# Optimization experiments

Measured on AMD Instinct MI355X. Metric: run time of the kernel, lower is better.

Reference implementation:

```python
import jax, jax.numpy as jnp
import numpy as np

B, C, IMG, P = 64, 3, 224, 16
GRID = IMG // P          # 14
N = GRID * GRID          # 196 patch tokens
D = 768
L, H = 12, 12
HD = D // H              # 64
FF = 4 * D               # 3072
NC = 1000
PRUNE_LAYER = 6
KEEP = max(1, int(N * 0.5))  # 98 tokens kept after pruning
LN_EPS = 1e-6


def _ln(x, g, b):
    m = jnp.mean(x, axis=-1, keepdims=True)
    v = jnp.var(x, axis=-1, keepdims=True)
    return (x - m) * jax.lax.rsqrt(v + LN_EPS) * g + b


def _block(x, g1, b1, qw, qb, pw, pb, g2, b2, w1, c1, w2, c2):
    # standard timm ViT block: x + Attn(LN(x)); x + MLP(LN(x))
    Bq, S, _ = x.shape
    h = _ln(x, g1, b1)
    qkv = (h @ qw + qb).reshape(Bq, S, 3, H, HD)
    q, k, v = qkv[:, :, 0], qkv[:, :, 1], qkv[:, :, 2]  # [B,S,H,HD]
    attn = jax.nn.softmax(jnp.einsum('bqhd,bkhd->bhqk', q, k) * (HD ** -0.5), axis=-1)
    o = jnp.einsum('bhqk,bkhd->bqhd', attn, v).reshape(Bq, S, D)
    x = x + o @ pw + pb
    h = _ln(x, g2, b2)
    return x + jax.nn.gelu(h @ w1 + c1, approximate=False) @ w2 + c2


def _forward(x, patch_w, patch_b, cls_token, pos_embed, ln1_g, ln1_b, qkv_w, qkv_b,
             proj_w, proj_b, ln2_g, ln2_b, fc1_w, fc1_b, fc2_w, fc2_b,
             norm_g, norm_b, head_w, head_b):
    Bq = x.shape[0]
    # patch embed: conv(k=16, s=16) == patchify + linear; flatten order (C, ph, pw) matches torch conv weight layout
    patches = x.reshape(Bq, C, GRID, P, GRID, P).transpose(0, 2, 4, 1, 3, 5).reshape(Bq, N, C * P * P)
    t = patches @ patch_w + patch_b                                     # [B,N,D]
    t = jnp.concatenate([jnp.broadcast_to(cls_token, (Bq, 1, D)), t], axis=1) + pos_embed  # [B,197,D]

    blk = lambda t, i: _block(t, ln1_g[i], ln1_b[i], qkv_w[i], qkv_b[i], proj_w[i], proj_b[i],
                              ln2_g[i], ln2_b[i], fc1_w[i], fc1_b[i], fc2_w[i], fc2_b[i])
    for i in range(PRUNE_LAYER):
        t = blk(t, i)

    cls_tok, patch_tok = t[:, :1], t[:, 1:]
    # per-token L2 scores + topk selection + gather (the irregular-access stage)
    scores = jnp.sqrt(jnp.sum(patch_tok * patch_tok, axis=-1))          # [B,N]
    _, idx = jax.lax.top_k(scores, KEEP)                                # sorted descending, matches torch.topk
    sel = jnp.take_along_axis(patch_tok, idx[:, :, None], axis=1)       # [B,K,D]
    t = jnp.concatenate([cls_tok, sel], axis=1)                         # [B,K+1,D]

    for i in range(PRUNE_LAYER, L):
        t = blk(t, i)
    t = _ln(t, norm_g, norm_b)
    return t[:, 0] @ head_w + head_b                                    # [B,NC]


def setup_inputs() -> dict:
    key = jax.random.key(0)
    ks = jax.random.split(key, 12)
    s = 0.02
    f32 = jnp.float32
    return {
        'x': jax.random.normal(ks[0], (B, C, IMG, IMG), f32),
        'patch_w': jax.random.normal(ks[1], (C * P * P, D), f32) * s,
        'patch_b': jnp.zeros((D,), f32),
        'cls_token': jax.random.normal(ks[2], (1, 1, D), f32) * s,
        'pos_embed': jax.random.normal(ks[3], (1, N + 1, D), f32) * s,
        'ln1_g': jnp.ones((L, D), f32), 'ln1_b': jnp.zeros((L, D), f32),
        'qkv_w': jax.random.normal(ks[4], (L, D, 3 * D), f32) * s,
        'qkv_b': jnp.zeros((L, 3 * D), f32),
        'proj_w': jax.random.normal(ks[5], (L, D, D), f32) * s,
        'proj_b': jnp.zeros((L, D), f32),
        'ln2_g': jnp.ones((L, D), f32), 'ln2_b': jnp.zeros((L, D), f32),
        'fc1_w': jax.random.normal(ks[6], (L, D, FF), f32) * s,
        'fc1_b': jnp.zeros((L, FF), f32),
        'fc2_w': jax.random.normal(ks[7], (L, FF, D), f32) * s,
        'fc2_b': jnp.zeros((L, D), f32),
        'norm_g': jnp.ones((D,), f32), 'norm_b': jnp.zeros((D,), f32),
        'head_w': jax.random.normal(ks[8], (D, NC), f32) * s,
        'head_b': jnp.zeros((NC,), f32),
    }


def reference(x, patch_w, patch_b, cls_token, pos_embed, ln1_g, ln1_b, qkv_w, qkv_b,
              proj_w, proj_b, ln2_g, ln2_b, fc1_w, fc1_b, fc2_w, fc2_b,
              norm_g, norm_b, head_w, head_b):
    return _forward(x, patch_w, patch_b, cls_token, pos_embed, ln1_g, ln1_b, qkv_w, qkv_b,
                    proj_w, proj_b, ln2_g, ln2_b, fc1_w, fc1_b, fc2_w, fc2_b,
                    norm_g, norm_b, head_w, head_b)
```

## Files before the change

kernel.cpp:

```cpp
#include <hip/hip_runtime.h>
#include <hip/hip_bf16.h>
#include <cstddef>
#include <cstdint>

namespace {

constexpr int B = 64, CIN = 3, IMG = 224, PS = 16, GRID_ = 14, NPATCH = 196;
constexpr int D = 768, H = 12, HD = 64, FFD = 3072, NC = 1000;
constexpr int S1 = 197, S2 = 99, KEEP = 98, PRUNE = 6, LAYERS = 12;
constexpr float LN_EPS = 1e-6f;

typedef __attribute__((ext_vector_type(8))) short bf16x8;
typedef __attribute__((ext_vector_type(4))) float f32x4;

__device__ inline float wave_red_sum(float v) {
  #pragma unroll
  for (int off = 32; off > 0; off >>= 1) v += __shfl_xor(v, off, 64);
  return v;
}

__device__ inline void gl16(const __hip_bfloat16* g, __hip_bfloat16* l) {
  __builtin_amdgcn_global_load_lds(
      (const __attribute__((address_space(1))) void*)g,
      (__attribute__((address_space(3))) void*)l,
      16, 0, 0);
}

__global__ __launch_bounds__(256) void tcvt_k(const float* __restrict__ src,
                                              __hip_bfloat16* __restrict__ dst,
                                              int R, int C, size_t lstride) {
  src += (size_t)blockIdx.z * lstride;
  dst += (size_t)blockIdx.z * lstride;
  __shared__ float tile[32][33];
  int c0 = blockIdx.x * 32, r0 = blockIdx.y * 32;
  int tx = threadIdx.x & 31, ty = threadIdx.x >> 5;
  #pragma unroll
  for (int i = 0; i < 32; i += 8) {
    int r = r0 + ty + i, c = c0 + tx;
    tile[ty + i][tx] = (r < R && c < C) ? src[(size_t)r * C + c] : 0.f;
  }
  __syncthreads();
  #pragma unroll
  for (int i = 0; i < 32; i += 8) {
    int c = c0 + ty + i, r = r0 + tx;
    if (c < C && r < R) dst[(size_t)c * R + r] = __float2bfloat16(tile[tx][ty + i]);
  }
}

__global__ void patchify_k(const float* __restrict__ x, __hip_bfloat16* __restrict__ out) {
  size_t idx = (size_t)blockIdx.x * blockDim.x + threadIdx.x;
  size_t total = (size_t)B * NPATCH * D;
  if (idx >= total) return;
  int row = (int)(idx / D), k = (int)(idx % D);
  int b = row / NPATCH, n = row % NPATCH;
  int gr = n / GRID_, gc = n % GRID_;
  int c = k / (PS * PS), rr = (k % (PS * PS)) / PS, cc = k % PS;
  out[idx] = __float2bfloat16(x[((size_t)(b * CIN + c) * IMG + (gr * PS + rr)) * IMG + gc * PS + cc]);
}

template <int MODE>
__global__ __launch_bounds__(256) void bgemm_k(
    const __hip_bfloat16* __restrict__ A, const __hip_bfloat16* __restrict__ BT,
    const float* __restrict__ bias, void* __restrict__ Cc,
    int M, int N, int K, const float* __restrict__ extra) {
  __shared__ __hip_bfloat16 As[128 * 32];
  __shared__ __hip_bfloat16 Bs[128 * 32];
  int tid = threadIdx.x, lane = tid & 63, wv = tid >> 6;
  int wr = wv >> 1, wc = wv & 1;
  int m0 = blockIdx.y * 128, n0 = blockIdx.x * 128;
  int fr = lane & 15, fq = lane >> 4;
  int srow0 = wv * 32 + (lane >> 2);
  int skk = (lane & 3) * 8;
  f32x4 acc[4][4] = {};
  for (int k0 = 0; k0 < K; k0 += 32) {
    #pragma unroll
    for (int i = 0; i < 2; ++i) {
      int r = srow0 + i * 16;
      int gra = m0 + r; gra = (gra < M) ? gra : (M - 1);
      gl16(A + (size_t)gra * K + k0 + skk, &As[r * 32 + skk]);
      int grb = n0 + r; grb = (grb < N) ? grb : (N - 1);
      gl16(BT + (size_t)grb * K + k0 + skk, &Bs[r * 32 + skk]);
    }
    __syncthreads();
    bf16x8 af[4], bg[4];
    #pragma unroll
    for (int m = 0; m < 4; ++m) af[m] = *(const bf16x8*)&As[(wr * 64 + m * 16 + fr) * 32 + fq * 8];
    #pragma unroll
    for (int n = 0; n < 4; ++n) bg[n] = *(const bf16x8*)&Bs[(wc * 64 + n * 16 + fr) * 32 + fq * 8];
    #pragma unroll
    for (int m = 0; m < 4; ++m)
      #pragma unroll
      for (int n = 0; n < 4; ++n)
        acc[m][n] = __builtin_amdgcn_mfma_f32_16x16x32_bf16(af[m], bg[n], acc[m][n], 0, 0, 0);
    __syncthreads();
  }
  #pragma unroll
  for (int m = 0; m < 4; ++m) {
    #pragma unroll
    for (int n = 0; n < 4; ++n) {
      #pragma unroll
      for (int j = 0; j < 4; ++j) {
        int row = m0 + wr * 64 + m * 16 + fq * 4 + j;
        int col = n0 + wc * 64 + n * 16 + fr;
        if (row >= M || col >= N) continue;
        float v = acc[m][n][j] + bias[col];
        if (MODE == 0) {
          ((__hip_bfloat16*)Cc)[(size_t)row * N + col] = __float2bfloat16(v);
        } else if (MODE == 1) {
          int b = row / NPATCH, nn = row % NPATCH;
          ((float*)Cc)[((size_t)(b * S1 + 1 + nn)) * D + col] = v + extra[(size_t)(1 + nn) * D + col];
        } else if (MODE == 2) {
          ((float*)Cc)[(size_t)row * N + col] += v;
        } else {
          float g = 0.5f * v * (1.0f + erff(v * 0.7071067811865476f));
          ((__hip_bfloat16*)Cc)[(size_t)row * N + col] = __float2bfloat16(g);
        }
      }
    }
  }
}

__global__ __launch_bounds__(256) void gemm_k(
    const float* __restrict__ A, const float* __restrict__ Bw,
    const float* __restrict__ bias, float* __restrict__ Cc,
    int M, int N, int K) {
  __shared__ float As[64][17];
  __shared__ float Bs[16][64];
  int tid = threadIdx.x;
  int tx = tid & 15, ty = tid >> 4;
  int m0 = blockIdx.y * 64, n0 = blockIdx.x * 64;
  float acc[4][4] = {};
  for (int k0 = 0; k0 < K; k0 += 16) {
    #pragma unroll
    for (int j = 0; j < 4; ++j) {
      int i = tid + 256 * j;
      int r = i >> 4, c = i & 15;
      int gr = m0 + r;
      As[r][c] = (gr < M) ? A[(size_t)gr * K + (k0 + c)] : 0.f;
    }
    #pragma unroll
    for (int j = 0; j < 4; ++j) {
      int i = tid + 256 * j;
      int r = i >> 6, c = i & 63;
      int gc = n0 + c;
      Bs[r][c] = (gc < N) ? Bw[(size_t)(k0 + r) * N + gc] : 0.f;
    }
    __syncthreads();
    #pragma unroll
    for (int kk = 0; kk < 16; ++kk) {
      float a[4], bb[4];
      #pragma unroll
      for (int ii = 0; ii < 4; ++ii) a[ii] = As[ty * 4 + ii][kk];
      #pragma unroll
      for (int jj = 0; jj < 4; ++jj) bb[jj] = Bs[kk][tx * 4 + jj];
      #pragma unroll
      for (int ii = 0; ii < 4; ++ii)
        #pragma unroll
        for (int jj = 0; jj < 4; ++jj) acc[ii][jj] = fmaf(a[ii], bb[jj], acc[ii][jj]);
    }
    __syncthreads();
  }
  #pragma unroll
  for (int ii = 0; ii < 4; ++ii) {
    int row = m0 + ty * 4 + ii;
    if (row >= M) continue;
    #pragma unroll
    for (int jj = 0; jj < 4; ++jj) {
      int col = n0 + tx * 4 + jj;
      if (col >= N) continue;
      Cc[(size_t)row * N + col] = acc[ii][jj] + bias[col];
    }
  }
}

__global__ void cls_init_k(float* __restrict__ t, const float* __restrict__ cls,
                           const float* __restrict__ pos) {
  int idx = blockIdx.x * blockDim.x + threadIdx.x;
  if (idx >= B * D) return;
  int b = idx / D, d = idx % D;
  t[(size_t)b * S1 * D + d] = cls[d] + pos[d];
}

template <typename OutT>
__global__ __launch_bounds__(256) void ln_k(const float* __restrict__ in, OutT* __restrict__ out,
                                            const float* __restrict__ g, const float* __restrict__ bta,
                                            size_t istride, size_t ostride) {
  int row = blockIdx.x;
  const float* p = in + (size_t)row * istride;
  int tid = threadIdx.x;
  float v0 = p[tid], v1 = p[tid + 256], v2 = p[tid + 512];
  float s = v0 + v1 + v2;
  float s2 = v0 * v0 + v1 * v1 + v2 * v2;
  s = wave_red_sum(s);
  s2 = wave_red_sum(s2);
  __shared__ float r1[4], r2[4];
  int lane = tid & 63, w = tid >> 6;
  if (lane == 0) { r1[w] = s; r2[w] = s2; }
  __syncthreads();
  s = r1[0] + r1[1] + r1[2] + r1[3];
  s2 = r2[0] + r2[1] + r2[2] + r2[3];
  float mean = s * (1.0f / 768.0f);
  float var = s2 * (1.0f / 768.0f) - mean * mean;
  float rs = rsqrtf(var + LN_EPS);
  OutT* q = out + (size_t)row * ostride;
  #pragma unroll
  for (int c = 0; c < 3; ++c) {
    int i = tid + 256 * c;
    float vv = (c == 0 ? v0 : (c == 1 ? v1 : v2));
    float r = (vv - mean) * rs * g[i] + bta[i];
    if constexpr (sizeof(OutT) == 2) q[i] = __float2bfloat16(r);
    else q[i] = r;
  }
}

template <int NT16>
__global__ __launch_bounds__(256) void attn3_k(const __hip_bfloat16* __restrict__ qkv,
                                               __hip_bfloat16* __restrict__ o, int S) {
  constexpr int NT32 = (NT16 + 1) / 2;
  constexpr int COLS = NT32 * 32;
  constexpr int STR = COLS + 8;
  __shared__ __hip_bfloat16 VT[64 * STR];
  __shared__ __hip_bfloat16 P[4][16 * STR];
  int bh = blockIdx.x;
  int b = bh / H, hh = bh % H;
  int tid = threadIdx.x, lane = tid & 63, wv = tid >> 6;
  int fr = lane & 15, fq = lane >> 4;
  const size_t rs = 3 * D;
  const __hip_bfloat16* qb = qkv + ((size_t)b * S) * rs + hh * HD;
  const __hip_bfloat16* kb = qb + D;
  const __hip_bfloat16* vb = qb + 2 * D;
  const __hip_bfloat16 z = __float2bfloat16(0.f);
  for (int idx = tid; idx < COLS * 64; idx += 256) {
    int key = idx >> 6, d = idx & 63;
    VT[d * STR + key] = (key < S) ? vb[(size_t)key * rs + d] : z;
  }
  if (NT16 & 1) {
    for (int idx = lane; idx < 16 * 16; idx += 64)
      P[wv][(idx >> 4) * STR + NT16 * 16 + (idx & 15)] = z;
  }
  __syncthreads();

  for (int qt = wv; qt * 16 < S; qt += 4) {
    int q0 = qt * 16;
    int qrow = q0 + fr;
    const __hip_bfloat16* qp = qb + (size_t)(qrow < S ? qrow : 0) * rs + fq * 8;
    bf16x8 aq0 = *(const bf16x8*)(qp);
    bf16x8 aq1 = *(const bf16x8*)(qp + 32);
    f32x4 sc[NT16];
    #pragma unroll
    for (int kt = 0; kt < NT16; ++kt) {
      int krow = kt * 16 + fr;
      const __hip_bfloat16* kp = kb + (size_t)(krow < S ? krow : 0) * rs + fq * 8;
      bf16x8 bk0 = *(const bf16x8*)(kp);
      bf16x8 bk1 = *(const bf16x8*)(kp + 32);
      f32x4 a = {};
      a = __builtin_amdgcn_mfma_f32_16x16x32_bf16(aq0, bk0, a, 0, 0, 0);
      a = __builtin_amdgcn_mfma_f32_16x16x32_bf16(aq1, bk1, a, 0, 0, 0);
      sc[kt] = a;
    }
    float lj[4];
    #pragma unroll
    for (int jj = 0; jj < 4; ++jj) {
      float mx = -1e30f;
      #pragma unroll
      for (int kt = 0; kt < NT16; ++kt) {
        float v = sc[kt][jj] * 0.125f;
        if (kt * 16 + fr >= S) v = -1e30f;
        sc[kt][jj] = v;
        mx = fmaxf(mx, v);
      }
      mx = fmaxf(mx, __shfl_xor(mx, 1, 64));
      mx = fmaxf(mx, __shfl_xor(mx, 2, 64));
      mx = fmaxf(mx, __shfl_xor(mx, 4, 64));
      mx = fmaxf(mx, __shfl_xor(mx, 8, 64));
      float sum = 0.f;
      #pragma unroll
      for (int kt = 0; kt < NT16; ++kt) {
        float p = __expf(sc[kt][jj] - mx);
        sc[kt][jj] = p;
        sum += p;
      }
      sum += __shfl_xor(sum, 1, 64);
      sum += __shfl_xor(sum, 2, 64);
      sum += __shfl_xor(sum, 4, 64);
      sum += __shfl_xor(sum, 8, 64);
      lj[jj] = 1.0f / sum;
    }
    __hip_bfloat16* pw = &P[wv][0];
    #pragma unroll
    for (int kt = 0; kt < NT16; ++kt)
      #pragma unroll
      for (int jj = 0; jj < 4; ++jj)
        pw[(fq * 4 + jj) * STR + kt * 16 + fr] = __float2bfloat16(sc[kt][jj]);
    #pragma unroll
    for (int dt = 0; dt < 4; ++dt) {
      f32x4 oa = {};
      #pragma unroll
      for (int kc = 0; kc < NT32; ++kc) {
        bf16x8 ap = *(const bf16x8*)&pw[fr * STR + kc * 32 + fq * 8];
        bf16x8 bv = *(const bf16x8*)&VT[(dt * 16 + fr) * STR + kc * 32 + fq * 8];
        oa = __builtin_amdgcn_mfma_f32_16x16x32_bf16(ap, bv, oa, 0, 0, 0);
      }
      #pragma unroll
      for (int jj = 0; jj < 4; ++jj) {
        int orow = q0 + fq * 4 + jj;
        if (orow < S)
          o[((size_t)(b * S + orow)) * D + hh * HD + dt * 16 + fr] =
              __float2bfloat16(oa[jj] * lj[jj]);
      }
    }
  }
}

__global__ void score_k(const float* __restrict__ t, float* __restrict__ scores) {
  int gw = (blockIdx.x * blockDim.x + threadIdx.x) >> 6;
  int lane = threadIdx.x & 63;
  if (gw >= B * NPATCH) return;
  int b = gw / NPATCH, n = gw % NPATCH;
  const float* p = t + ((size_t)(b * S1) + 1 + n) * D;
  float a = 0.f;
  #pragma unroll
  for (int j = lane; j < D; j += 64) { float v = p[j]; a += v * v; }
  a = wave_red_sum(a);
  if (lane == 0) scores[gw] = sqrtf(a);
}

__global__ __launch_bounds__(256) void select_k(const float* __restrict__ scores, int* __restrict__ map) {
  int b = blockIdx.x;
  __shared__ float s[NPATCH];
  __shared__ int flag[NPATCH];
  int i = threadIdx.x;
  if (i < NPATCH) s[i] = scores[b * NPATCH + i];
  __syncthreads();
  if (i < NPATCH) {
    float si = s[i];
    int r = 0;
    for (int j = 0; j < NPATCH; ++j) {
      float sj = s[j];
      r += (sj > si) || (sj == si && j < i);
    }
    flag[i] = (r < KEEP) ? 1 : 0;
  }
  __syncthreads();
  if (i < NPATCH && flag[i]) {
    int p = 0;
    for (int j = 0; j < i; ++j) p += flag[j];
    map[b * (KEEP + 1) + 1 + p] = 1 + i;
  }
  if (i == 0) map[b * (KEEP + 1)] = 0;
}

__global__ void gather_k(const float* __restrict__ t, const int* __restrict__ map,
                         float* __restrict__ t2) {
  int br = blockIdx.x;
  int b = br / S2;
  int src = map[br];
  const float* p = t + ((size_t)b * S1 + src) * D;
  float* q = t2 + (size_t)br * D;
  for (int j = threadIdx.x; j < D; j += blockDim.x) q[j] = p[j];
}

}

extern "C" void kernel_launch(void* const* d_in, const int* in_sizes, int n_in,
                              void* d_out, int out_size, void* d_ws, size_t ws_size,
                              hipStream_t stream) {
  const float* x       = (const float*)d_in[0];
  const float* patch_w = (const float*)d_in[1];
  const float* patch_b = (const float*)d_in[2];
  const float* cls_tok = (const float*)d_in[3];
  const float* pos_emb = (const float*)d_in[4];
  const float* ln1_g   = (const float*)d_in[5];
  const float* ln1_b   = (const float*)d_in[6];
  const float* qkv_w   = (const float*)d_in[7];
  const float* qkv_b   = (const float*)d_in[8];
  const float* proj_w  = (const float*)d_in[9];
  const float* proj_b  = (const float*)d_in[10];
  const float* ln2_g   = (const float*)d_in[11];
  const float* ln2_b   = (const float*)d_in[12];
  const float* fc1_w   = (const float*)d_in[13];
  const float* fc1_b   = (const float*)d_in[14];
  const float* fc2_w   = (const float*)d_in[15];
  const float* fc2_b   = (const float*)d_in[16];
  const float* norm_g  = (const float*)d_in[17];
  const float* norm_b  = (const float*)d_in[18];
  const float* head_w  = (const float*)d_in[19];
  const float* head_b  = (const float*)d_in[20];
  float* out = (float*)d_out;

  char* wp = (char*)d_ws;
  auto alloc = [&](size_t bytes) { char* r = wp; wp += (bytes + 255) & ~(size_t)255; return r; };
  float* t   = (float*)alloc((size_t)B * S1 * D * 4);
  float* t2  = (float*)alloc((size_t)B * S2 * D * 4);
  float* hf  = (float*)alloc((size_t)B * D * 4);
  float* scores = (float*)alloc((size_t)B * NPATCH * 4);
  int*   map    = (int*)alloc((size_t)B * S2 * 4);
  __hip_bfloat16* h   = (__hip_bfloat16*)alloc((size_t)B * S1 * D * 2);
  __hip_bfloat16* qkv = (__hip_bfloat16*)alloc((size_t)B * S1 * 3 * D * 2);
  __hip_bfloat16* ff  = (__hip_bfloat16*)alloc((size_t)B * S1 * FFD * 2);
  __hip_bfloat16* qkvT  = (__hip_bfloat16*)alloc((size_t)LAYERS * 3 * D * D * 2);
  __hip_bfloat16* projT = (__hip_bfloat16*)alloc((size_t)LAYERS * D * D * 2);
  __hip_bfloat16* fc1T  = (__hip_bfloat16*)alloc((size_t)LAYERS * FFD * D * 2);
  __hip_bfloat16* fc2T  = (__hip_bfloat16*)alloc((size_t)LAYERS * D * FFD * 2);
  __hip_bfloat16* patchT = (__hip_bfloat16*)alloc((size_t)D * D * 2);
  __hip_bfloat16* patches = ff;

  { dim3 g(3 * D / 32, D / 32, LAYERS);
    tcvt_k<<<g, 256, 0, stream>>>(qkv_w, qkvT, D, 3 * D, (size_t)D * 3 * D); }
  { dim3 g(D / 32, D / 32, LAYERS);
    tcvt_k<<<g, 256, 0, stream>>>(proj_w, projT, D, D, (size_t)D * D); }
  { dim3 g(FFD / 32, D / 32, LAYERS);
    tcvt_k<<<g, 256, 0, stream>>>(fc1_w, fc1T, D, FFD, (size_t)D * FFD); }
  { dim3 g(D / 32, FFD / 32, LAYERS);
    tcvt_k<<<g, 256, 0, stream>>>(fc2_w, fc2T, FFD, D, (size_t)FFD * D); }
  { dim3 g(D / 32, D / 32, 1);
    tcvt_k<<<g, 256, 0, stream>>>(patch_w, patchT, D, D, 0); }

  {
    size_t total = (size_t)B * NPATCH * D;
    patchify_k<<<(unsigned)((total + 255) / 256), 256, 0, stream>>>(x, patches);
    dim3 g(D / 128, (B * NPATCH) / 128);
    bgemm_k<1><<<g, 256, 0, stream>>>(patches, patchT, patch_b, t, B * NPATCH, D, D, pos_emb);
    cls_init_k<<<(B * D + 255) / 256, 256, 0, stream>>>(t, cls_tok, pos_emb);
  }

  auto run_block = [&](float* tb, int S, int l) {
    int M = B * S;
    int mb = (M + 127) / 128;
    ln_k<__hip_bfloat16><<<M, 256, 0, stream>>>(tb, h, ln1_g + (size_t)l * D, ln1_b + (size_t)l * D, D, D);
    { dim3 g(3 * D / 128, mb);
      bgemm_k<0><<<g, 256, 0, stream>>>(h, qkvT + (size_t)l * 3 * D * D, qkv_b + (size_t)l * 3 * D,
                                        qkv, M, 3 * D, D, nullptr); }
    if (S == S1) attn3_k<13><<<B * H, 256, 0, stream>>>(qkv, h, S);
    else         attn3_k<7><<<B * H, 256, 0, stream>>>(qkv, h, S);
    { dim3 g(D / 128, mb);
      bgemm_k<2><<<g, 256, 0, stream>>>(h, projT + (size_t)l * D * D, proj_b + (size_t)l * D,
                                        tb, M, D, D, nullptr); }
    ln_k<__hip_bfloat16><<<M, 256, 0, stream>>>(tb, h, ln2_g + (size_t)l * D, ln2_b + (size_t)l * D, D, D);
    { dim3 g(FFD / 128, mb);
      bgemm_k<3><<<g, 256, 0, stream>>>(h, fc1T + (size_t)l * FFD * D, fc1_b + (size_t)l * FFD,
                                        ff, M, FFD, D, nullptr); }
    { dim3 g(D / 128, mb);
      bgemm_k<2><<<g, 256, 0, stream>>>(ff, fc2T + (size_t)l * D * FFD, fc2_b + (size_t)l * D,
                                        tb, M, D, FFD, nullptr); }
  };

  for (int l = 0; l < PRUNE; ++l) run_block(t, S1, l);

  score_k<<<(B * NPATCH * 64 + 255) / 256, 256, 0, stream>>>(t, scores);
  select_k<<<B, 256, 0, stream>>>(scores, map);
  gather_k<<<B * S2, 256, 0, stream>>>(t, map, t2);

  for (int l = PRUNE; l < LAYERS; ++l) run_block(t2, S2, l);

  ln_k<float><<<B, 256, 0, stream>>>(t2, hf, norm_g, norm_b, (size_t)S2 * D, D);
  { dim3 g((NC + 63) / 64, (B + 63) / 64);
    gemm_k<<<g, 256, 0, stream>>>(hf, head_w, head_b, out, B, NC, D); }
}
```

Baseline: 5.268 ms.

## Double-buffer GEMM LDS tiles and XOR-swizzle LDS layout

The bf16 MFMA GEMM now keeps two LDS buffers per operand. The next K-tile is issued with global_load_lds before the MFMAs on the current tile run, so the global load latency can overlap with compute. The LDS layout is also XOR-swizzled on 16-byte chunks, chosen by row, and the fragment reads are adjusted to match; this is meant to cut LDS bank conflicts. The cost is twice the LDS per block, which can lower occupancy, and the barrier's wait on outstanding loads may still limit how much overlap is achieved.

```diff
diff --git a/kernel.cpp b/kernel.cpp
--- a/kernel.cpp
+++ b/kernel.cpp
@@ -63,30 +63,42 @@
     const __hip_bfloat16* __restrict__ A, const __hip_bfloat16* __restrict__ BT,
     const float* __restrict__ bias, void* __restrict__ Cc,
     int M, int N, int K, const float* __restrict__ extra) {
-  __shared__ __hip_bfloat16 As[128 * 32];
-  __shared__ __hip_bfloat16 Bs[128 * 32];
+  __shared__ __hip_bfloat16 As[2][128 * 32];
+  __shared__ __hip_bfloat16 Bs[2][128 * 32];
   int tid = threadIdx.x, lane = tid & 63, wv = tid >> 6;
   int wr = wv >> 1, wc = wv & 1;
   int m0 = blockIdx.y * 128, n0 = blockIdx.x * 128;
   int fr = lane & 15, fq = lane >> 4;
-  int srow0 = wv * 32 + (lane >> 2);
-  int skk = (lane & 3) * 8;
+  int srow = lane >> 2;
+  int scd = (lane & 3) ^ ((lane >> 3) & 3);
+  int rswz = (fq ^ ((fr >> 1) & 3)) * 8;
+  int nk = K >> 5;
+
+  auto stage = [&](int buf, int kt) {
+    int k0 = kt << 5;
+    #pragma unroll
+    for (int i = 0; i < 2; ++i) {
+      int r = wv * 32 + i * 16 + srow;
+      int gra = m0 + r; gra = (gra < M) ? gra : (M - 1);
+      gl16(A + (size_t)gra * K + k0 + scd * 8, &As[buf][(wv * 32 + i * 16) * 32]);
+      int grb = n0 + r; grb = (grb < N) ? grb : (N - 1);
+      gl16(BT + (size_t)grb * K + k0 + scd * 8, &Bs[buf][(wv * 32 + i * 16) * 32]);
+    }
+  };
+
   f32x4 acc[4][4] = {};
-  for (int k0 = 0; k0 < K; k0 += 32) {
-    #pragma unroll
-    for (int i = 0; i < 2; ++i) {
-      int r = srow0 + i * 16;
-      int gra = m0 + r; gra = (gra < M) ? gra : (M - 1);
-      gl16(A + (size_t)gra * K + k0 + skk, &As[r * 32 + skk]);
-      int grb = n0 + r; grb = (grb < N) ? grb : (N - 1);
-      gl16(BT + (size_t)grb * K + k0 + skk, &Bs[r * 32 + skk]);
-    }
-    __syncthreads();
+  stage(0, 0);
+  __syncthreads();
+  for (int kt = 0; kt < nk; ++kt) {
+    int buf = kt & 1;
+    if (kt + 1 < nk) stage(buf ^ 1, kt + 1);
     bf16x8 af[4], bg[4];
     #pragma unroll
-    for (int m = 0; m < 4; ++m) af[m] = *(const bf16x8*)&As[(wr * 64 + m * 16 + fr) * 32 + fq * 8];
-    #pragma unroll
-    for (int n = 0; n < 4; ++n) bg[n] = *(const bf16x8*)&Bs[(wc * 64 + n * 16 + fr) * 32 + fq * 8];
+    for (int m = 0; m < 4; ++m)
+      af[m] = *(const bf16x8*)&As[buf][(wr * 64 + m * 16 + fr) * 32 + rswz];
+    #pragma unroll
+    for (int n = 0; n < 4; ++n)
+      bg[n] = *(const bf16x8*)&Bs[buf][(wc * 64 + n * 16 + fr) * 32 + rswz];
     #pragma unroll
     for (int m = 0; m < 4; ++m)
       #pragma unroll
```

New measurement: 5.028 ms. -4.6%, faster.
